# Kernel optimization log

Hardware: AMD Instinct MI355X
Metric: run time of the kernel (lower is better)

Reference implementation:

```python
import math
import jax, jax.numpy as jnp
import numpy as np

N_HEADS = 16
HEAD_DIM = 128
NUM_BUCKETS = 32
MAX_DISTANCE = 128
ROPE_BASE = 10000.0


def _rope_cos_sin(seq_len, head_dim, dtype):
    inv_freq = 1.0 / (ROPE_BASE ** (jnp.arange(0, head_dim, 2, dtype=jnp.float32) / head_dim))
    ang = jnp.arange(seq_len, dtype=jnp.float32)[:, None] * inv_freq[None, :]  # [S, hd/2]
    return jnp.cos(ang).astype(dtype), jnp.sin(ang).astype(dtype)


def _apply_rope(t, cos, sin):
    # t: [B, S, H, D] (NeoX rotate-half); cos/sin: [S, D/2]
    d2 = t.shape[-1] // 2
    t1, t2 = t[..., :d2], t[..., d2:]
    c = cos[None, :, None, :]
    s = sin[None, :, None, :]
    return jnp.concatenate([t1 * c - t2 * s, t2 * c + t1 * s], axis=-1)


def _relative_bucket(q_len, k_len):
    # unidirectional (causal) T5 bucketing: relative_position = 0 - min(mem - ctx, 0)
    ctx = jnp.arange(q_len, dtype=jnp.int32)[:, None]
    mem = jnp.arange(k_len, dtype=jnp.int32)[None, :]
    n = jnp.maximum(ctx - mem, 0)  # [Q, K]
    max_exact = NUM_BUCKETS // 2
    is_small = n < max_exact
    nf = jnp.maximum(n, 1).astype(jnp.float32)
    large = (jnp.log(nf / max_exact) / math.log(MAX_DISTANCE / max_exact)
             * (NUM_BUCKETS - max_exact)).astype(jnp.int32) + max_exact
    large = jnp.minimum(large, NUM_BUCKETS - 1)
    return jnp.where(is_small, n, large)


def setup_inputs() -> dict:
    key = jax.random.key(0)
    k1, k2, k3, k4 = jax.random.split(key, 4)
    B, S, H = 2, 2048, 2048
    return {
        "x": jax.random.normal(k1, (B, S, H), jnp.float32),
        "qkv_w": jax.random.normal(k2, (H, 3 * H), jnp.float32) * 0.02,
        "dense_w": jax.random.normal(k3, (H, H), jnp.float32) * 0.02,
        "rel_attn_table": jax.random.normal(k4, (NUM_BUCKETS, N_HEADS), jnp.float32) * 0.1,
    }


def reference(x, qkv_w, dense_w, rel_attn_table):
    B, S, H = x.shape
    qkv = x @ qkv_w                         # [B, S, 3H]
    q, k, v = jnp.split(qkv, 3, axis=-1)
    q = q.reshape(B, S, N_HEADS, HEAD_DIM)
    k = k.reshape(B, S, N_HEADS, HEAD_DIM)
    v = v.reshape(B, S, N_HEADS, HEAD_DIM)

    cos, sin = _rope_cos_sin(S, HEAD_DIM, x.dtype)
    q = _apply_rope(q, cos, sin)
    k = _apply_rope(k, cos, sin)

    scale = 1.0 / math.sqrt(HEAD_DIM)       # q_scaling = 1.0
    scores = jnp.einsum("bqhd,bkhd->bhqk", q, k) * scale  # [B, nH, S, S]

    # T5 relative position bias: embedding(bucket, table).permute(2,0,1) -> [1, nH, S, S]
    bucket = _relative_bucket(S, S)
    bias = rel_attn_table[bucket]            # [S, S, nH]
    scores = scores + jnp.transpose(bias, (2, 0, 1))[None]

    # causal mask (make_causal_mask): key index > query index -> large negative
    causal = jnp.tril(jnp.ones((S, S), dtype=bool))
    neg = jnp.asarray(jnp.finfo(x.dtype).min, x.dtype)
    scores = jnp.where(causal[None, None], scores, neg)

    probs = jax.nn.softmax(scores, axis=-1)
    ctx = jnp.einsum("bhqk,bkhd->bqhd", probs, v).reshape(B, S, H)
    return ctx @ dense_w
```

## Files before the change

### kernel.cpp

```cpp
#include <hip/hip_runtime.h>

typedef unsigned short u16;
typedef __bf16 bf16_t;
typedef __bf16 bf16x8 __attribute__((ext_vector_type(8)));
typedef float f32x4 __attribute__((ext_vector_type(4)));
typedef unsigned short u16x8 __attribute__((ext_vector_type(8)));
typedef unsigned short u16x4 __attribute__((ext_vector_type(4)));

#define S_LEN 2048
#define NHEAD 16
#define HD 128
#define HID 2048
#define QKV_N 6144

__device__ __forceinline__ float b2f(u16 u) {
  union { unsigned int i; float f; } x; x.i = ((unsigned int)u) << 16; return x.f;
}
__device__ __forceinline__ u16 f2b(float f) {
  bf16_t h = (bf16_t)f;
  return __builtin_bit_cast(unsigned short, h);
}

__device__ __forceinline__ void gl_lds16(const u16* g, u16* l) {
  __builtin_amdgcn_global_load_lds(
      (const __attribute__((address_space(1))) unsigned int*)g,
      (__attribute__((address_space(3))) unsigned int*)l, 16, 0, 0);
}

__global__ void detect_dtype_k(const void* __restrict__ x, int* __restrict__ flag) {
  __shared__ int cnt;
  if (threadIdx.x == 0) cnt = 0;
  __syncthreads();
  const u16* xu = (const u16*)x;
  int sane = 0;
  for (int i = threadIdx.x; i < 8192; i += 256) {
    int e = (xu[i] >> 7) & 0xFF;
    if (e == 0 || (e > 100 && e < 140)) sane++;
  }
  atomicAdd(&cnt, sane);
  __syncthreads();
  if (threadIdx.x == 0) *flag = (cnt < 7373) ? 1 : 0;
}

__global__ __launch_bounds__(256) void convert_any_k(const void* __restrict__ in, u16* __restrict__ out,
                                                     const int* __restrict__ flag) {
  int i = (blockIdx.x * 256 + threadIdx.x) * 4;
  if (*flag) {
    const float4 v = *(const float4*)((const float*)in + i);
    u16x4 o = {f2b(v.x), f2b(v.y), f2b(v.z), f2b(v.w)};
    *(u16x4*)(out + i) = o;
  } else {
    *(u16x4*)(out + i) = *(const u16x4*)((const u16*)in + i);
  }
}

__global__ __launch_bounds__(256) void transpose_any(const void* __restrict__ in,
                                                     u16* __restrict__ out, int R, int C,
                                                     const int* __restrict__ flag) {
  __shared__ u16 t[64][65];
  bool isf = (*flag != 0);
  int tid = threadIdx.x;
  int r0 = blockIdx.y * 64, c0 = blockIdx.x * 64;
#pragma unroll
  for (int p = 0; p < 16; ++p) {
    int e = p * 256 + tid;
    int r = e >> 6, c = e & 63;
    size_t idx = (size_t)(r0 + r) * C + (c0 + c);
    t[r][c] = isf ? f2b(((const float*)in)[idx]) : ((const u16*)in)[idx];
  }
  __syncthreads();
#pragma unroll
  for (int p = 0; p < 16; ++p) {
    int e = p * 256 + tid;
    int r = e >> 6, c = e & 63;
    out[(size_t)(c0 + r) * R + (r0 + c)] = t[c][r];
  }
}

__global__ void rope_table_k(float* __restrict__ tab) {
  int i = blockIdx.x * 256 + threadIdx.x;
  int s = i >> 6, d = i & 63;
  float inv = expf(-(float)d * (9.210340371976184f / 64.0f));
  float ang = (float)s * inv;
  tab[s * 128 + d] = cosf(ang);
  tab[s * 128 + 64 + d] = sinf(ang);
}

__global__ void build_bias_k(const void* __restrict__ table, float* __restrict__ bias,
                             const int* __restrict__ flag) {
  int i = blockIdx.x * 256 + threadIdx.x;
  int h = i >> 11, dist = i & 2047;
  int bucket;
  if (dist < 16) bucket = dist;
  else {
    int lb = (int)(logf((float)dist * 0.0625f) / 2.0794415f * 16.0f) + 16;
    bucket = lb < 31 ? lb : 31;
  }
  int ti = bucket * NHEAD + h;
  float tv = (*flag) ? ((const float*)table)[ti] : b2f(((const u16*)table)[ti]);
  bias[h * 2048 + dist] = tv;
}

template <bool F32OUT>
__global__ __launch_bounds__(256) void gemm_bt(const u16* __restrict__ A, const u16* __restrict__ B,
                                               void* __restrict__ Cv, int M, int N, int K) {
  __shared__ __align__(16) u16 As[128 * 32];
  __shared__ __align__(16) u16 Bs[128 * 32];
  int tid = threadIdx.x;
  int lane = tid & 63, wv = tid >> 6;
  int wm = wv & 1, wn = wv >> 1;
  int lane16 = lane & 15, quad = lane >> 4;
  int m0 = blockIdx.y * 128, n0 = blockIdx.x * 128;

  const u16* pA = A + (size_t)(m0 + wv * 32 + (lane >> 2)) * K + (lane & 3) * 8;
  const u16* pB = B + (size_t)(n0 + wv * 32 + (lane >> 2)) * K + (lane & 3) * 8;
  u16* lA = As + wv * 1024;
  u16* lB = Bs + wv * 1024;

  f32x4 zero4 = {0.f, 0.f, 0.f, 0.f};
  f32x4 acc[4][4];
#pragma unroll
  for (int i = 0; i < 4; ++i)
#pragma unroll
    for (int j = 0; j < 4; ++j) acc[i][j] = zero4;

  int nk = K >> 5;
  for (int kt = 0; kt < nk; ++kt) {
    __syncthreads();
    gl_lds16(pA, lA);
    gl_lds16(pA + (size_t)16 * K, lA + 512);
    gl_lds16(pB, lB);
    gl_lds16(pB + (size_t)16 * K, lB + 512);
    pA += 32; pB += 32;
    __syncthreads();
    bf16x8 af[4], bfr[4];
#pragma unroll
    for (int i = 0; i < 4; ++i)
      af[i] = *(const bf16x8*)&As[(wm * 64 + i * 16 + lane16) * 32 + quad * 8];
#pragma unroll
    for (int j = 0; j < 4; ++j)
      bfr[j] = *(const bf16x8*)&Bs[(wn * 64 + j * 16 + lane16) * 32 + quad * 8];
#pragma unroll
    for (int i = 0; i < 4; ++i)
#pragma unroll
      for (int j = 0; j < 4; ++j)
        acc[i][j] = __builtin_amdgcn_mfma_f32_16x16x32_bf16(af[i], bfr[j], acc[i][j], 0, 0, 0);
  }
#pragma unroll
  for (int i = 0; i < 4; ++i)
#pragma unroll
    for (int j = 0; j < 4; ++j)
#pragma unroll
      for (int r = 0; r < 4; ++r) {
        int row = m0 + wm * 64 + i * 16 + quad * 4 + r;
        int col = n0 + wn * 64 + j * 16 + lane16;
        if (F32OUT)
          ((float*)Cv)[(size_t)row * N + col] = acc[i][j][r];
        else
          ((u16*)Cv)[(size_t)row * N + col] = f2b(acc[i][j][r]);
      }
}

template <bool F32OUT>
__global__ __launch_bounds__(512, 2) void gemm256_bt(const u16* __restrict__ A,
                                                     const u16* __restrict__ B,
                                                     void* __restrict__ Cv,
                                                     int M, int N, int K) {
  __shared__ __align__(16) u16 sA[2][16384];
  __shared__ __align__(16) u16 sB[2][16384];
  (void)M;
  const int tid = threadIdx.x;
  const int lane = tid & 63, w = tid >> 6;
  const int wm = w >> 2, wn = w & 3;
  const int lane16 = lane & 15, quad = lane >> 4;

  const int nbx = gridDim.x;
  const int nwg = nbx * gridDim.y;
  const int bid = blockIdx.y * nbx + blockIdx.x;
  const int cpx = nwg >> 3;
  const int swz = (bid & 7) * cpx + (bid >> 3);
  const int m0 = (swz / nbx) * 256;
  const int n0 = (swz % nbx) * 256;

  const int rl = lane >> 2;
  const int ch = (lane & 3) ^ (((lane >> 5) & 1) << 1);
  const u16* pA_ = A + (size_t)(m0 + w * 16 + rl) * K + ch * 8;
  const u16* pB_ = B + (size_t)(n0 + w * 16 + rl) * K + ch * 8;

  const int fro = lane16 * 32 + ((quad * 8) ^ ((lane16 & 8) << 1));

  f32x4 zero4 = {0.f, 0.f, 0.f, 0.f};
  f32x4 acc[8][4];
#pragma unroll
  for (int i = 0; i < 8; ++i)
#pragma unroll
    for (int j = 0; j < 4; ++j) acc[i][j] = zero4;

  bf16x8 af[4][2];
  bf16x8 bfr[4][2];

#define STAGE_A(BUF, H, KO)                                      \
  do {                                                           \
    const u16* _s = pA_ + (size_t)(H) * 128 * K + (KO);          \
    u16* _d = &sA[BUF][(H) * 8192 + w * 1024];                   \
    gl_lds16(_s, _d);                                            \
    gl_lds16(_s + 32, _d + 512);                                 \
  } while (0)
#define STAGE_B(BUF, H, KO)                                      \
  do {                                                           \
    const u16* _s = pB_ + (size_t)(H) * 128 * K + (KO);          \
    u16* _d = &sB[BUF][(H) * 8192 + w * 1024];                   \
    gl_lds16(_s, _d);                                            \
    gl_lds16(_s + 32, _d + 512);                                 \
  } while (0)
#define READ_A(BUF, MH)                                                              \
  _Pragma("unroll") for (int i = 0; i < 4; ++i)                                      \
  _Pragma("unroll") for (int ks = 0; ks < 2; ++ks)                                   \
    af[i][ks] = *(const bf16x8*)&sA[BUF][((wm * 8 + (MH) * 4 + i) * 2 + ks) * 512 + fro];
#define READ_B(BUF, NH)                                                              \
  _Pragma("unroll") for (int j = 0; j < 2; ++j)                                      \
  _Pragma("unroll") for (int ks = 0; ks < 2; ++ks)                                   \
    bfr[(NH) * 2 + j][ks] = *(const bf16x8*)&sB[BUF][((wn * 4 + (NH) * 2 + j) * 2 + ks) * 512 + fro];
#define MFMA_Q(MH, NH)                                                               \
  __builtin_amdgcn_s_setprio(1);                                                     \
  _Pragma("unroll") for (int i = 0; i < 4; ++i)                                      \
  _Pragma("unroll") for (int j = 0; j < 2; ++j)                                      \
  _Pragma("unroll") for (int ks = 0; ks < 2; ++ks)                                   \
    acc[(MH) * 4 + i][(NH) * 2 + j] = __builtin_amdgcn_mfma_f32_16x16x32_bf16(       \
        af[i][ks], bfr[(NH) * 2 + j][ks], acc[(MH) * 4 + i][(NH) * 2 + j], 0, 0, 0); \
  __builtin_amdgcn_s_setprio(0);
#define GBAR() __builtin_amdgcn_s_barrier()
#define VMCNT4() asm volatile("s_waitcnt vmcnt(4)" ::: "memory")

  STAGE_A(0, 0, 0); STAGE_A(0, 1, 0);
  STAGE_B(0, 0, 0); STAGE_B(0, 1, 0);
  STAGE_B(1, 0, 64); STAGE_A(1, 0, 64);
  VMCNT4();
  GBAR();

  const int nIt = K >> 7;
  for (int it = 0; it < nIt; ++it) {
    int k1 = (it << 7) + 64;
    int k2 = k1 + 64; if (k2 >= K) k2 = 0;
    int k3 = k2 + 64; if (k3 >= K) k3 = 0;
    READ_A(0, 0); READ_B(0, 0);
    STAGE_A(1, 1, k1);
    GBAR(); MFMA_Q(0, 0); GBAR();
    READ_B(0, 1);
    STAGE_B(1, 1, k1);
    GBAR(); MFMA_Q(0, 1); GBAR();
    READ_A(0, 1);
    STAGE_B(0, 0, k2);
    GBAR(); MFMA_Q(1, 1); GBAR();
    STAGE_A(0, 0, k2);
    GBAR(); MFMA_Q(1, 0); VMCNT4(); GBAR();
    READ_A(1, 0); READ_B(1, 0);
    STAGE_A(0, 1, k2);
    GBAR(); MFMA_Q(0, 0); GBAR();
    READ_B(1, 1);
    STAGE_B(0, 1, k2);
    GBAR(); MFMA_Q(0, 1); GBAR();
    READ_A(1, 1);
    STAGE_B(1, 0, k3);
    GBAR(); MFMA_Q(1, 1); GBAR();
    STAGE_A(1, 0, k3);
    GBAR(); MFMA_Q(1, 0); VMCNT4(); GBAR();
  }
  asm volatile("s_waitcnt vmcnt(0)" ::: "memory");

#pragma unroll
  for (int i = 0; i < 8; ++i)
#pragma unroll
    for (int j = 0; j < 4; ++j)
#pragma unroll
      for (int r = 0; r < 4; ++r) {
        int row = m0 + wm * 128 + i * 16 + quad * 4 + r;
        int col = n0 + wn * 64 + j * 16 + lane16;
        if (F32OUT)
          ((float*)Cv)[(size_t)row * N + col] = acc[i][j][r];
        else
          ((u16*)Cv)[(size_t)row * N + col] = f2b(acc[i][j][r]);
      }
#undef STAGE_A
#undef STAGE_B
#undef READ_A
#undef READ_B
#undef MFMA_Q
#undef GBAR
#undef VMCNT4
}

__global__ __launch_bounds__(256) void reorg_k(const u16* __restrict__ qkv, const float* __restrict__ tab,
                                               u16* __restrict__ q, u16* __restrict__ k,
                                               u16* __restrict__ vT) {
  __shared__ float vt[64][129];
  int tid = threadIdx.x;
  int st = blockIdx.x, bh = blockIdx.y;
  int b = bh >> 4, h = bh & 15;
  int s0 = st * 64;
  const u16* base = qkv + (size_t)(b * S_LEN + s0) * QKV_N + h * HD;
  u16* qo = q + ((size_t)bh * S_LEN + s0) * HD;
  u16* ko = k + ((size_t)bh * S_LEN + s0) * HD;
#pragma unroll
  for (int p = 0; p < 16; ++p) {
    int e = p * 256 + tid;
    int sl = e >> 6, d = e & 63;
    float c = tab[(s0 + sl) * 128 + d];
    float sn = tab[(s0 + sl) * 128 + 64 + d];
    const u16* rowp = base + (size_t)sl * QKV_N;
    float q1 = b2f(rowp[d]), q2 = b2f(rowp[d + 64]);
    qo[sl * HD + d] = f2b(q1 * c - q2 * sn);
    qo[sl * HD + d + 64] = f2b(q2 * c + q1 * sn);
    float k1 = b2f(rowp[2048 + d]), k2 = b2f(rowp[2048 + d + 64]);
    ko[sl * HD + d] = f2b(k1 * c - k2 * sn);
    ko[sl * HD + d + 64] = f2b(k2 * c + k1 * sn);
  }
#pragma unroll
  for (int p = 0; p < 32; ++p) {
    int e = p * 256 + tid;
    int sl = e >> 7, d = e & 127;
    vt[sl][d] = b2f(base[(size_t)sl * QKV_N + 4096 + d]);
  }
  __syncthreads();
  u16* vo = vT + (size_t)bh * HD * S_LEN;
#pragma unroll
  for (int p = 0; p < 32; ++p) {
    int e = p * 256 + tid;
    int d = e >> 6, sl = e & 63;
    vo[(size_t)d * S_LEN + s0 + sl] = f2b(vt[sl][d]);
  }
}

__global__ __launch_bounds__(256) void attn_k(const u16* __restrict__ q, const u16* __restrict__ k,
                                              const u16* __restrict__ vT, const float* __restrict__ bias,
                                              u16* __restrict__ ctx) {
  __shared__ __align__(16) u16 Ks[64 * 128];
  __shared__ __align__(16) u16 VTs[128 * 64];
  __shared__ __align__(16) u16 QP[64 * 128];
  __shared__ float bias_s[128];
  int tid = threadIdx.x;
  int lane = tid & 63, wq = tid >> 6;
  int lane16 = lane & 15, quad = lane >> 4;
  int r7 = lane16 & 7;
  int bh = blockIdx.y;
  int b = bh >> 4, h = bh & 15;
  const u16* kg = k + (size_t)bh * S_LEN * HD;
  const u16* vg = vT + (size_t)bh * HD * S_LEN;
  const float* biasr = bias + h * 2048;
  const float scale = 0.08838834764831845f;
  f32x4 zero4 = {0.f, 0.f, 0.f, 0.f};

  int rl4 = lane >> 4, pk = lane & 15;
  int rl8 = lane >> 3, pv = lane & 7;
  u16* Pw = QP + wq * 1152;

  for (int half = 0; half < 2; ++half) {
    int qt = half ? (31 - blockIdx.x) : blockIdx.x;
    int q0 = qt * 64;
    const u16* qg = q + ((size_t)bh * S_LEN + q0) * HD;

    __syncthreads();
    {
      int r = tid >> 4, c = (tid & 15) * 8;
#pragma unroll
      for (int p = 0; p < 4; ++p)
        *(u16x8*)&QP[(r + p * 16) * 128 + c] = *(const u16x8*)&qg[(size_t)(r + p * 16) * HD + c];
    }
    __syncthreads();
    bf16x8 qf[4];
#pragma unroll
    for (int kd = 0; kd < 4; ++kd)
      qf[kd] = *(const bf16x8*)&QP[(wq * 16 + lane16) * 128 + kd * 32 + quad * 8];
    __syncthreads();

    float m_i[4], l_i[4];
    f32x4 o[8];
#pragma unroll
    for (int r = 0; r < 4; ++r) { m_i[r] = -1e30f; l_i[r] = 0.f; }
#pragma unroll
    for (int dt = 0; dt < 8; ++dt) o[dt] = zero4;

    for (int kt = 0; kt <= qt; ++kt) {
      int k0 = kt * 64;
      if (kt) __syncthreads();
#pragma unroll
      for (int t = 0; t < 4; ++t) {
        int g = wq * 4 + t;
        int rowk = g * 4 + rl4;
        int ck = (pk & 8) | ((pk & 7) ^ (rowk & 7));
        gl_lds16(kg + (size_t)(k0 + rowk) * HD + ck * 8, Ks + g * 512);
        int rowv = g * 8 + rl8;
        int cv = pv ^ (rowv & 7);
        gl_lds16(vg + (size_t)rowv * S_LEN + k0 + cv * 8, VTs + g * 512);
      }
      if (tid < 128) {
        int dist = q0 - k0 + tid - 64;
        bias_s[tid] = (dist >= 0) ? biasr[dist] : 0.f;
      }
      __syncthreads();

      f32x4 sc[4];
#pragma unroll
      for (int j = 0; j < 4; ++j) sc[j] = zero4;
#pragma unroll
      for (int kd = 0; kd < 4; ++kd)
#pragma unroll
        for (int j = 0; j < 4; ++j) {
          int cd = kd * 4 + quad;
          int pos = (cd & 8) | ((cd & 7) ^ r7);
          bf16x8 kf = *(const bf16x8*)&Ks[(j * 16 + lane16) * 128 + pos * 8];
          sc[j] = __builtin_amdgcn_mfma_f32_16x16x32_bf16(qf[kd], kf, sc[j], 0, 0, 0);
        }

      int qrel = wq * 16 + quad * 4;
#pragma unroll
      for (int j = 0; j < 4; ++j) {
        int krel = j * 16 + lane16;
#pragma unroll
        for (int r = 0; r < 4; ++r) {
          bool valid = (q0 + qrel + r) >= (k0 + krel);
          float sv = sc[j][r] * scale + bias_s[64 + (qrel + r) - krel];
          sc[j][r] = valid ? sv : -1e30f;
        }
      }
      float mx[4];
#pragma unroll
      for (int r = 0; r < 4; ++r)
        mx[r] = fmaxf(fmaxf(sc[0][r], sc[1][r]), fmaxf(sc[2][r], sc[3][r]));
#pragma unroll
      for (int xm = 1; xm < 16; xm <<= 1)
#pragma unroll
        for (int r = 0; r < 4; ++r) mx[r] = fmaxf(mx[r], __shfl_xor(mx[r], xm));
      float alpha[4];
#pragma unroll
      for (int r = 0; r < 4; ++r) {
        float mn = fmaxf(m_i[r], mx[r]);
        alpha[r] = __expf(m_i[r] - mn);
        m_i[r] = mn;
      }
#pragma unroll
      for (int j = 0; j < 4; ++j)
#pragma unroll
        for (int r = 0; r < 4; ++r) sc[j][r] = __expf(sc[j][r] - m_i[r]);
      float rs[4];
#pragma unroll
      for (int r = 0; r < 4; ++r) rs[r] = (sc[0][r] + sc[1][r]) + (sc[2][r] + sc[3][r]);
#pragma unroll
      for (int xm = 1; xm < 16; xm <<= 1)
#pragma unroll
        for (int r = 0; r < 4; ++r) rs[r] += __shfl_xor(rs[r], xm);
#pragma unroll
      for (int r = 0; r < 4; ++r) l_i[r] = l_i[r] * alpha[r] + rs[r];
#pragma unroll
      for (int dt = 0; dt < 8; ++dt)
#pragma unroll
        for (int r = 0; r < 4; ++r) o[dt][r] *= alpha[r];

#pragma unroll
      for (int j = 0; j < 4; ++j)
#pragma unroll
        for (int r = 0; r < 4; ++r)
          Pw[(quad * 4 + r) * 72 + j * 16 + lane16] = f2b(sc[j][r]);
      __threadfence_block();

#pragma unroll
      for (int ks = 0; ks < 2; ++ks) {
        bf16x8 pf = *(const bf16x8*)&Pw[lane16 * 72 + ks * 32 + quad * 8];
#pragma unroll
        for (int dt = 0; dt < 8; ++dt) {
          int cdv = ks * 4 + quad;
          int posv = cdv ^ r7;
          bf16x8 vf = *(const bf16x8*)&VTs[(dt * 16 + lane16) * 64 + posv * 8];
          o[dt] = __builtin_amdgcn_mfma_f32_16x16x32_bf16(pf, vf, o[dt], 0, 0, 0);
        }
      }
    }
#pragma unroll
    for (int r = 0; r < 4; ++r) {
      float invl = 1.0f / l_i[r];
      int srow = q0 + wq * 16 + quad * 4 + r;
      u16* orow = ctx + ((size_t)b * S_LEN + srow) * HID + h * HD;
#pragma unroll
      for (int dt = 0; dt < 8; ++dt)
        orow[dt * 16 + lane16] = f2b(o[dt][r] * invl);
    }
  }
}

extern "C" void kernel_launch(void* const* d_in, const int* in_sizes, int n_in,
                              void* d_out, int out_size, void* d_ws, size_t ws_size,
                              hipStream_t stream) {
  const void* x       = d_in[0];
  const void* qkv_w   = d_in[1];
  const void* dense_w = d_in[2];
  const void* rtable  = d_in[3];
  char* ws = (char*)d_ws;

  int*   flag  = (int*)(ws);
  float* bias  = (float*)(ws + 256);
  float* tab   = (float*)(ws + 131328);
  u16*   wdT   = (u16*)(ws + 1179904);
  u16*   vT    = (u16*)(ws + 9568512);
  u16*   x_bf  = (u16*)(ws + 26345728);
  u16*   qA    = x_bf;
  u16*   wqkvT = (u16*)(ws + 43122944);
  u16*   kA    = wqkvT;
  u16*   qkv   = (u16*)(ws + 68288768);
  u16*   ctx   = qkv;

  detect_dtype_k<<<1, 256, 0, stream>>>(x, flag);
  convert_any_k<<<8192, 256, 0, stream>>>(x, x_bf, flag);
  transpose_any<<<dim3(96, 32), 256, 0, stream>>>(qkv_w, wqkvT, 2048, 6144, flag);
  transpose_any<<<dim3(32, 32), 256, 0, stream>>>(dense_w, wdT, 2048, 2048, flag);
  rope_table_k<<<512, 256, 0, stream>>>(tab);
  build_bias_k<<<128, 256, 0, stream>>>(rtable, bias, flag);
  gemm256_bt<false><<<dim3(24, 16), 512, 0, stream>>>(x_bf, wqkvT, qkv, 4096, 6144, 2048);
  reorg_k<<<dim3(32, 32), 256, 0, stream>>>(qkv, tab, qA, kA, vT);
  attn_k<<<dim3(16, 32), 256, 0, stream>>>(qA, kA, vT, bias, ctx);
  gemm_bt<true><<<dim3(16, 32), 256, 0, stream>>>(ctx, wdT, d_out, 4096, 2048, 2048);
}
```

Before: 463.0 us.

## Restructure GEMM prefetch schedule to stage whole buffers ahead

Changes the GEMM main loop's global-to-LDS staging so each LDS buffer is loaded in full (both halves of A and B) one buffer ahead, instead of interleaving half-buffer loads for the next k-step. The prologue now preloads both buffers completely, and the wait allows 8 outstanding loads instead of 4. The aim is a deeper prefetch window that hides global memory latency better. The cost is bursts of staging clustered in the back half of each buffer's compute phase, which may contend with the MFMA work at those points.

```diff
diff --git a/kernel.cpp b/kernel.cpp
--- a/kernel.cpp
+++ b/kernel.cpp
@@ -230,41 +230,38 @@
         af[i][ks], bfr[(NH) * 2 + j][ks], acc[(MH) * 4 + i][(NH) * 2 + j], 0, 0, 0); \
   __builtin_amdgcn_s_setprio(0);
 #define GBAR() __builtin_amdgcn_s_barrier()
-#define VMCNT4() asm volatile("s_waitcnt vmcnt(4)" ::: "memory")
+#define VMCNT8() asm volatile("s_waitcnt vmcnt(8)" ::: "memory")
 
   STAGE_A(0, 0, 0); STAGE_A(0, 1, 0);
   STAGE_B(0, 0, 0); STAGE_B(0, 1, 0);
-  STAGE_B(1, 0, 64); STAGE_A(1, 0, 64);
-  VMCNT4();
+  STAGE_B(1, 0, 64); STAGE_B(1, 1, 64);
+  STAGE_A(1, 0, 64); STAGE_A(1, 1, 64);
+  VMCNT8();
   GBAR();
 
   const int nIt = K >> 7;
   for (int it = 0; it < nIt; ++it) {
-    int k1 = (it << 7) + 64;
-    int k2 = k1 + 64; if (k2 >= K) k2 = 0;
-    int k3 = k2 + 64; if (k3 >= K) k3 = 0;
+    int base = it << 7;
+    int k2 = base + 128; if (k2 >= K) k2 = 0;
+    int k3 = base + 192; if (k3 >= K) k3 = 0;
     READ_A(0, 0); READ_B(0, 0);
-    STAGE_A(1, 1, k1);
     GBAR(); MFMA_Q(0, 0); GBAR();
     READ_B(0, 1);
-    STAGE_B(1, 1, k1);
     GBAR(); MFMA_Q(0, 1); GBAR();
     READ_A(0, 1);
-    STAGE_B(0, 0, k2);
+    STAGE_B(0, 0, k2); STAGE_B(0, 1, k2);
     GBAR(); MFMA_Q(1, 1); GBAR();
-    STAGE_A(0, 0, k2);
-    GBAR(); MFMA_Q(1, 0); VMCNT4(); GBAR();
+    STAGE_A(0, 0, k2); STAGE_A(0, 1, k2);
+    GBAR(); MFMA_Q(1, 0); VMCNT8(); GBAR();
     READ_A(1, 0); READ_B(1, 0);
-    STAGE_A(0, 1, k2);
     GBAR(); MFMA_Q(0, 0); GBAR();
     READ_B(1, 1);
-    STAGE_B(0, 1, k2);
     GBAR(); MFMA_Q(0, 1); GBAR();
     READ_A(1, 1);
-    STAGE_B(1, 0, k3);
+    STAGE_B(1, 0, k3); STAGE_B(1, 1, k3);
     GBAR(); MFMA_Q(1, 1); GBAR();
-    STAGE_A(1, 0, k3);
-    GBAR(); MFMA_Q(1, 0); VMCNT4(); GBAR();
+    STAGE_A(1, 0, k3); STAGE_A(1, 1, k3);
+    GBAR(); MFMA_Q(1, 0); VMCNT8(); GBAR();
   }
   asm volatile("s_waitcnt vmcnt(0)" ::: "memory");
 
@@ -287,7 +284,7 @@
 #undef READ_B
 #undef MFMA_Q
 #undef GBAR
-#undef VMCNT4
+#undef VMCNT8
 }
 
 __global__ __launch_bounds__(256) void reorg_k(const u16* __restrict__ qkv, const float* __restrict__ tab,
```

New measurement: 464.9 us. Within noise of the previous version (+0.4%).
